# Kernel optimization log

Measured on AMD Instinct MI355X. Metric: run time of the kernel, lower is better.

The kernel has to match this reference:

```python
import jax, jax.numpy as jnp
import numpy as np

N = 100000   # nodes
E = 400000   # edges
G = 5000     # graphs (20 nodes each)
H = 128      # hidden_channels
ATOM_D, BOND_D, BOOL_D = 16, 8, 2
NODE_D = 30 + ATOM_D + 3 * BOOL_D   # 52
EDGE_D = 2 + BOND_D + 3 * BOOL_D    # 16


def setup_inputs() -> dict:
    key = jax.random.key(0)
    ks = jax.random.split(key, 24)
    rn = lambda k, shape: jax.random.normal(k, shape, dtype=jnp.float32) * 0.05
    # node features: [atom_idx, 10 continuous, 3 bools]
    atom_idx = jax.random.randint(ks[0], (N,), 1, 119)
    node_cont = jax.random.normal(ks[1], (N, 10), dtype=jnp.float32)
    node_bool = jax.random.randint(ks[2], (N, 3), 0, 2)
    x = jnp.concatenate([atom_idx[:, None].astype(jnp.float32), node_cont,
                         node_bool.astype(jnp.float32)], axis=1)
    # edge features: [bond_idx, 1 continuous, 3 bools]
    bond_idx = jax.random.randint(ks[3], (E,), 1, 22)
    edge_cont = jax.random.normal(ks[4], (E, 1), dtype=jnp.float32)
    edge_bool = jax.random.randint(ks[5], (E, 3), 0, 2)
    edge_attr = jnp.concatenate([bond_idx[:, None].astype(jnp.float32), edge_cont,
                                 edge_bool.astype(jnp.float32)], axis=1)
    edge_index = jax.random.randint(ks[6], (2, E), 0, N)
    batch = jnp.repeat(jnp.arange(G, dtype=jnp.int32), N // G)
    # embeddings (with padding rows zeroed, as nn.Embedding padding_idx)
    atom_emb = rn(ks[7], (119, ATOM_D)).at[0].set(0.0)
    bond_emb = rn(ks[8], (22, BOND_D)).at[0].set(0.0)
    bool_emb = rn(ks[9], (3, BOOL_D)).at[2].set(0.0)
    Wn = rn(ks[10], (10, 30)); bn = jnp.zeros((30,), jnp.float32)
    We = rn(ks[11], (1, 2));   be = jnp.zeros((2,), jnp.float32)
    Wl1 = rn(ks[12], (NODE_D, H)); bl1 = jnp.zeros((H,), jnp.float32)
    Wr1 = rn(ks[13], (NODE_D, H)); br1 = jnp.zeros((H,), jnp.float32)
    Wedge1 = rn(ks[14], (EDGE_D, H)); att1 = rn(ks[15], (H,))
    bias1 = jnp.zeros((H,), jnp.float32)
    Wl2 = rn(ks[16], (H, H)); bl2 = jnp.zeros((H,), jnp.float32)
    Wr2 = rn(ks[17], (H, H)); br2 = jnp.zeros((H,), jnp.float32)
    Wedge2 = rn(ks[18], (EDGE_D, H)); att2 = rn(ks[19], (H,))
    bias2 = jnp.zeros((H,), jnp.float32)
    return dict(x=x, edge_index=edge_index, edge_attr=edge_attr, batch=batch,
                atom_emb=atom_emb, bond_emb=bond_emb, bool_emb=bool_emb,
                Wn=Wn, bn=bn, We=We, be=be,
                Wl1=Wl1, bl1=bl1, Wr1=Wr1, br1=br1, Wedge1=Wedge1, att1=att1, bias1=bias1,
                Wl2=Wl2, bl2=bl2, Wr2=Wr2, br2=br2, Wedge2=Wedge2, att2=att2, bias2=bias2)


def _gatv2(h, src, dst, e_lin, Wl, bl, Wr, br, att, bias):
    # PyG GATv2Conv, heads=1: xl = lin_l(x) (source), xr = lin_r(x) (target)
    xl = h @ Wl + bl
    xr = h @ Wr + br
    m = xl[src] + xr[dst] + e_lin                      # [E', H]
    a = jax.nn.leaky_relu(m, 0.2) @ att                # [E']
    amax = jax.ops.segment_max(a, dst, num_segments=N)
    ex = jnp.exp(a - amax[dst])
    denom = jax.ops.segment_sum(ex, dst, num_segments=N)
    alpha = ex / denom[dst]                            # softmax over incoming edges
    out = jax.ops.segment_sum(alpha[:, None] * xl[src], dst, num_segments=N)
    return out + bias


def reference(x, edge_index, edge_attr, batch,
              atom_emb, bond_emb, bool_emb, Wn, bn, We, be,
              Wl1, bl1, Wr1, br1, Wedge1, att1, bias1,
              Wl2, bl2, Wr2, br2, Wedge2, att2, bias2):
    # --- encode nodes ---
    ai = x[:, 0].astype(jnp.int32)
    nb = x[:, 11:14].astype(jnp.int32)
    h = jnp.concatenate([atom_emb[ai], x[:, 1:11] @ Wn + bn,
                         bool_emb[nb[:, 0]], bool_emb[nb[:, 1]], bool_emb[nb[:, 2]]], axis=1)
    # --- encode edges ---
    bi = edge_attr[:, 0].astype(jnp.int32)
    eb = edge_attr[:, 2:5].astype(jnp.int32)
    e = jnp.concatenate([bond_emb[bi], edge_attr[:, 1:2] @ We + be,
                         bool_emb[eb[:, 0]], bool_emb[eb[:, 1]], bool_emb[eb[:, 2]]], axis=1)
    src, dst = edge_index[0], edge_index[1]
    # --- add self loops with fill_value='mean' (mean of in-edge attrs per node) ---
    cnt = jax.ops.segment_sum(jnp.ones((E,), h.dtype), dst, num_segments=N)
    loop_attr = jax.ops.segment_sum(e, dst, num_segments=N) / jnp.maximum(cnt, 1.0)[:, None]
    e_full = jnp.concatenate([e, loop_attr], axis=0)          # [E+N, EDGE_D]
    loop = jnp.arange(N, dtype=src.dtype)
    src_f = jnp.concatenate([src, loop])
    dst_f = jnp.concatenate([dst, loop])
    # --- 3 GATv2 layers (layers 2 and 3 share weights, as in the original) ---
    h = jax.nn.relu(_gatv2(h, src_f, dst_f, e_full @ Wedge1, Wl1, bl1, Wr1, br1, att1, bias1))
    e_lin2 = e_full @ Wedge2
    h = jax.nn.relu(_gatv2(h, src_f, dst_f, e_lin2, Wl2, bl2, Wr2, br2, att2, bias2))
    h = jax.nn.relu(_gatv2(h, src_f, dst_f, e_lin2, Wl2, bl2, Wr2, br2, att2, bias2))
    # --- global_max_pool readout ---
    return jax.ops.segment_max(h, batch, num_segments=G)
```

## Files before the change

### kernel.cpp

```cpp
#include <hip/hip_runtime.h>
#include <hip/hip_fp16.h>

#define N_NODES 100000
#define N_EDGES 400000
#define N_GRAPHS 5000
#define NPG 20
#define SCAN_NB 256
#define SCAN_CHUNK ((N_NODES + SCAN_NB - 1) / SCAN_NB)
#define TAB_STRIDE (256 * 128 + 128)
#define F1 8192
#define F2 16384
#define NB_ENC ((N_NODES + 255) / 256)
#define NB_HIST ((N_EDGES + 255) / 256)

typedef __attribute__((ext_vector_type(8))) _Float16 f16x8;
typedef __attribute__((ext_vector_type(2))) _Float16 h2;
typedef __attribute__((ext_vector_type(4))) float f32x4;

#define DPP_QUAD_XOR1 0xB1
#define DPP_QUAD_XOR2 0x4E
#define DPP_ROW_HALF_MIRROR 0x141
#define DPP_ROW_MIRROR 0x140
template <int CTRL>
__device__ __forceinline__ float dpp_add(float x) {
  int p = __builtin_amdgcn_update_dpp(0, __float_as_int(x), CTRL, 0xf, 0xf, true);
  return x + __int_as_float(p);
}

__global__ __launch_bounds__(256) void k_prologue(
    const float* __restrict__ x, const float* __restrict__ atom_emb,
    const float* __restrict__ bool_emb, const float* __restrict__ Wn,
    const float* __restrict__ bn, __half* __restrict__ h0,
    const int* __restrict__ dst, int* __restrict__ cnt,
    const float* __restrict__ Wedge1, const float* __restrict__ Wedge2,
    const float* __restrict__ bond_emb, const float* __restrict__ We,
    const float* __restrict__ be, __half* __restrict__ tabs,
    const float* __restrict__ Wl1, const float* __restrict__ Wr1,
    const float* __restrict__ Wl2, const float* __restrict__ Wr2,
    unsigned short* __restrict__ fr, int* __restrict__ ghist) {
  int b = blockIdx.x, tid = threadIdx.x;
  if (b < NB_ENC) {
    int n = b * 256 + tid;
    if (n >= N_NODES) return;
    const float* xr = x + (size_t)n * 14;
    int ai = (int)xr[0];
    _Float16 hr[64];
    #pragma unroll
    for (int j = 0; j < 16; j++) hr[j] = (_Float16)atom_emb[ai * 16 + j];
    float xc[10];
    #pragma unroll
    for (int k = 0; k < 10; k++) xc[k] = xr[1 + k];
    #pragma unroll
    for (int c = 0; c < 30; c++) {
      float s = bn[c];
      #pragma unroll
      for (int k = 0; k < 10; k++) s += xc[k] * Wn[k * 30 + c];
      hr[16 + c] = (_Float16)s;
    }
    #pragma unroll
    for (int t = 0; t < 3; t++) {
      int bb = (int)xr[11 + t];
      hr[46 + 2 * t]     = (_Float16)bool_emb[2 * bb];
      hr[46 + 2 * t + 1] = (_Float16)bool_emb[2 * bb + 1];
    }
    #pragma unroll
    for (int j = 52; j < 64; j++) hr[j] = (_Float16)0.0f;
    uint4* d4 = (uint4*)(h0 + (size_t)n * 64);
    const uint4* s4 = (const uint4*)hr;
    #pragma unroll
    for (int j = 0; j < 8; j++) d4[j] = s4[j];
  } else if (b < NB_ENC + NB_HIST) {
    int e = (b - NB_ENC) * 256 + tid;
    if (e >= N_EDGES) return;
    atomicAdd(cnt + dst[e], 1);
  } else if (b == NB_ENC + NB_HIST) {
    if (tid < 64) ghist[tid] = 0;
    int s = tid >> 7, c = tid & 127;
    const float* W = s ? Wedge2 : Wedge1;
    __half* T12 = tabs + (size_t)s * TAB_STRIDE;
    __half* v   = T12 + 256 * 128;
    float w8 = W[8 * 128 + c], w9 = W[9 * 128 + c];
    v[c] = __float2half(We[0] * w8 + We[1] * w9);
    float cst = be[0] * w8 + be[1] * w9;
    float bond[22];
    for (int bb = 0; bb < 22; bb++) {
      float acc = 0.f;
      #pragma unroll
      for (int k = 0; k < 8; k++) acc += bond_emb[bb * 8 + k] * W[k * 128 + c];
      bond[bb] = acc;
    }
    for (int combo = 0; combo < 8; combo++) {
      float t2 = cst;
      #pragma unroll
      for (int tt = 0; tt < 3; tt++) {
        int bt = (combo >> tt) & 1;
        t2 += bool_emb[bt * 2 + 0] * W[(10 + 2 * tt + 0) * 128 + c];
        t2 += bool_emb[bt * 2 + 1] * W[(10 + 2 * tt + 1) * 128 + c];
      }
      for (int bb = 0; bb < 22; bb++)
        T12[(combo * 32 + bb) * 128 + c] = __float2half(bond[bb] + t2);
      for (int bb = 22; bb < 32; bb++)
        T12[(combo * 32 + bb) * 128 + c] = __float2half(0.f);
    }
  } else {
    int g = (b - (NB_ENC + NB_HIST + 1)) * 256 + tid;
    const float* W; int K; unsigned short* base; int fl;
    if (g < 1024)      { W = Wl1; K = 52;  base = fr;               fl = g; }
    else if (g < 2048) { W = Wr1; K = 52;  base = fr + F1;          fl = g - 1024; }
    else if (g < 4096) { W = Wl2; K = 128; base = fr + 2 * F1;      fl = g - 2048; }
    else if (g < 6144) { W = Wr2; K = 128; base = fr + 2 * F1 + F2; fl = g - 4096; }
    else return;
    int l = fl & 63, ctn = fl >> 6;
    int tn = ctn & 7, c = ctn >> 3;
    int n = tn * 16 + (l & 15);
    int kb = c * 32 + (l >> 4) * 8;
    unsigned h8[8];
    #pragma unroll
    for (int j = 0; j < 8; j++) {
      int k = kb + j;
      float v = (k < K) ? W[(size_t)k * 128 + n] : 0.f;
      __half hv = __float2half(v);
      h8[j] = (unsigned)*(unsigned short*)&hv;
    }
    uint4 hv4 = make_uint4(h8[0] | (h8[1] << 16), h8[2] | (h8[3] << 16),
                           h8[4] | (h8[5] << 16), h8[6] | (h8[7] << 16));
    *(uint4*)(base + (size_t)fl * 8) = hv4;
  }
}

__global__ __launch_bounds__(256) void k_scan1(const int* __restrict__ cnt,
                                               int* __restrict__ bsum,
                                               int* __restrict__ ghist) {
  __shared__ int red[256];
  __shared__ int lh[64];
  int b = blockIdx.x, t = threadIdx.x;
  if (t < 64) lh[t] = 0;
  __syncthreads();
  int beg = b * SCAN_CHUNK;
  int end = beg + SCAN_CHUNK; if (end > N_NODES) end = N_NODES;
  int s = 0;
  for (int i = beg + t; i < end; i += 256) {
    int cv = cnt[i];
    s += cv + 1;
    atomicAdd(&lh[cv < 63 ? cv : 63], 1);
  }
  red[t] = s;
  __syncthreads();
  for (int off = 128; off > 0; off >>= 1) {
    if (t < off) red[t] += red[t + off];
    __syncthreads();
  }
  if (t == 0) bsum[b] = red[0];
  if (t < 64 && lh[t] > 0) atomicAdd(&ghist[t], lh[t]);
}

__global__ __launch_bounds__(256) void k_scan3(const int* __restrict__ cnt,
                                               const int* __restrict__ bsum,
                                               int* __restrict__ indptr,
                                               int* __restrict__ cursor,
                                               const int* __restrict__ ghist,
                                               int* __restrict__ gcur) {
  __shared__ int sh[256];
  __shared__ int carry;
  int b = blockIdx.x, t = threadIdx.x;
  sh[t] = bsum[t];
  __syncthreads();
  for (int off = 1; off < 256; off <<= 1) {
    int v = (t >= off) ? sh[t - off] : 0;
    __syncthreads();
    sh[t] += v;
    __syncthreads();
  }
  if (t == 0) carry = (b > 0) ? sh[b - 1] : 0;
  __syncthreads();
  int beg = b * SCAN_CHUNK;
  int end = beg + SCAN_CHUNK; if (end > N_NODES) end = N_NODES;
  for (int base = beg; base < end; base += 256) {
    int i = base + t;
    int v = (i < end) ? cnt[i] + 1 : 0;
    sh[t] = v;
    __syncthreads();
    for (int off = 1; off < 256; off <<= 1) {
      int u = (t >= off) ? sh[t - off] : 0;
      __syncthreads();
      sh[t] += u;
      __syncthreads();
    }
    int excl = sh[t] - v;
    if (i < end) {
      int val = carry + excl;
      indptr[i] = val;
      cursor[i] = val;
    }
    __syncthreads();
    if (t == 255) carry += sh[255];
    __syncthreads();
  }
  if (b == 0 && t == 0) indptr[N_NODES] = N_EDGES + N_NODES;
  if (b == 0) {
    __syncthreads();
    if (t < 64) sh[t] = ghist[t];
    __syncthreads();
    if (t == 0) {
      int run = 0;
      for (int i = 0; i < 64; i++) { int v = sh[i]; sh[i] = run; run += v; }
    }
    __syncthreads();
    if (t < 64) gcur[t] = sh[t];
  }
}

__global__ void k_fill(const int* __restrict__ srcA,
                       const int* __restrict__ dst,
                       const float* __restrict__ eattr,
                       int* __restrict__ cursor,
                       int2* __restrict__ scode,
                       const int* __restrict__ cnt,
                       int* __restrict__ gcur,
                       int* __restrict__ perm) {
  int b = blockIdx.x, t = threadIdx.x;
  if (b < NB_HIST) {
    int e = b * 256 + t;
    if (e >= N_EDGES) return;
    const float* r = eattr + (size_t)e * 5;
    int bi = (int)r[0];
    float ec = r[1];
    int combo = (int)r[2] + 2 * (int)r[3] + 4 * (int)r[4];
    unsigned meta = (unsigned)(bi | (combo << 5));
    __half hec = __float2half(ec);
    meta |= ((unsigned)*(unsigned short*)&hec) << 16;
    int d = dst[e];
    int p = atomicAdd(&cursor[d], 1);
    scode[p] = make_int2(srcA[e], (int)meta);
  } else {
    __shared__ int lh[64];
    __shared__ int lbase[64];
    if (t < 64) lh[t] = 0;
    __syncthreads();
    int n = (b - NB_HIST) * 256 + t;
    bool v = (n < N_NODES);
    int dc = 0, r = 0;
    if (v) {
      int cv = cnt[n];
      dc = cv < 63 ? cv : 63;
      r = atomicAdd(&lh[dc], 1);
    }
    __syncthreads();
    if (t < 64 && lh[t] > 0) lbase[t] = atomicAdd(&gcur[t], lh[t]);
    __syncthreads();
    if (v) perm[lbase[dc] + r] = n;
  }
}

template <int KPAD>
__global__ __launch_bounds__(256, 4) void k_gemm2m(const __half* __restrict__ A,
                                                   const unsigned short* __restrict__ WfL,
                                                   const unsigned short* __restrict__ WfR,
                                                   const float* __restrict__ bl_,
                                                   const float* __restrict__ br_,
                                                   __half* __restrict__ outl,
                                                   __half* __restrict__ outr) {
  __shared__ unsigned short Bs[2][8192];
  const int tid = threadIdx.x;
  const int wv = tid >> 6, lane = tid & 63;
  const int tw = blockIdx.x * 4 + wv;
  const bool active = (tw < N_NODES / 16);
  const int ml = lane & 15, q = lane >> 4;
  const int m0 = active ? tw * 16 : 0;
  f32x4 accL[8], accR[8];
  #pragma unroll
  for (int t = 0; t < 8; t++) {
    accL[t] = (f32x4){0.f, 0.f, 0.f, 0.f};
    accR[t] = (f32x4){0.f, 0.f, 0.f, 0.f};
  }
  const _Float16* ar0 = (const _Float16*)A + (size_t)(m0 + ml) * KPAD + q * 8;
  constexpr int NC2 = KPAD / 64;
  for (int c2 = 0; c2 < NC2; c2++) {
    #pragma unroll
    for (int i0 = 0; i0 < 1024; i0 += 256) {
      int i = i0 + tid;
      size_t g = ((size_t)c2 * 1024 + i) * 8;
      *(uint4*)(&Bs[0][i * 8]) = *(const uint4*)(WfL + g);
      *(uint4*)(&Bs[1][i * 8]) = *(const uint4*)(WfR + g);
    }
    __syncthreads();
    #pragma unroll
    for (int sub = 0; sub < 2; sub++) {
      f16x8 a = *(const f16x8*)(ar0 + c2 * 64 + sub * 32);
      #pragma unroll
      for (int t = 0; t < 8; t++) {
        int idx = (sub * 512 + t * 64 + lane) * 8;
        f16x8 bL = *(const f16x8*)(&Bs[0][idx]);
        f16x8 bR = *(const f16x8*)(&Bs[1][idx]);
        accL[t] = __builtin_amdgcn_mfma_f32_16x16x32_f16(a, bL, accL[t], 0, 0, 0);
        accR[t] = __builtin_amdgcn_mfma_f32_16x16x32_f16(a, bR, accR[t], 0, 0, 0);
      }
    }
    __syncthreads();
  }
  __syncthreads();
  if (!active) return;
  __half* eb = (__half*)&Bs[0][0] + wv * 2048;
  const int srow = q * 4;
  const int rrow0 = lane >> 4;
  const int rcol = (lane & 15) * 8;
  #pragma unroll
  for (int t = 0; t < 8; t++) {
    int n = t * 16 + ml;
    float bL = bl_[n];
    #pragma unroll
    for (int r = 0; r < 4; r++)
      eb[(srow + r) * 128 + n] = __float2half(accL[t][r] + bL);
  }
  #pragma unroll
  for (int pp = 0; pp < 4; pp++) {
    uint4 v = *(const uint4*)(eb + pp * 512 + lane * 8);
    *(uint4*)(outl + (size_t)(m0 + pp * 4 + rrow0) * 128 + rcol) = v;
  }
  #pragma unroll
  for (int t = 0; t < 8; t++) {
    int n = t * 16 + ml;
    float bR = br_[n];
    #pragma unroll
    for (int r = 0; r < 4; r++)
      eb[(srow + r) * 128 + n] = __float2half(accR[t][r] + bR);
  }
  #pragma unroll
  for (int pp = 0; pp < 4; pp++) {
    uint4 v = *(const uint4*)(eb + pp * 512 + lane * 8);
    *(uint4*)(outr + (size_t)(m0 + pp * 4 + rrow0) * 128 + rcol) = v;
  }
}

__global__ __launch_bounds__(256) void k_gat(const __half* __restrict__ xl,
                                             const __half* __restrict__ xr,
                                             const int* __restrict__ indptr,
                                             const int2* __restrict__ scode,
                                             const __half* __restrict__ tabs,
                                             const float* __restrict__ att,
                                             const float* __restrict__ bias,
                                             __half* __restrict__ hout,
                                             const int* __restrict__ perm) {
  int wid = (blockIdx.x * 256 + threadIdx.x) >> 6;
  int nw = (gridDim.x * 256) >> 6;
  int lane = threadIdx.x & 63;
  int q4 = lane >> 4;
  int c = (lane & 15) * 8;
  const __half* T12 = tabs;
  uint4 vu_ = *(const uint4*)(tabs + 256 * 128 + c);
  h2 v4[4] = {*reinterpret_cast<h2*>(&vu_.x), *reinterpret_cast<h2*>(&vu_.y),
              *reinterpret_cast<h2*>(&vu_.z), *reinterpret_cast<h2*>(&vu_.w)};
  float4 af0 = *(const float4*)(att + c);
  float4 af1 = *(const float4*)(att + c + 4);
  h2 a4[4] = {{(_Float16)af0.x, (_Float16)af0.y}, {(_Float16)af0.z, (_Float16)af0.w},
              {(_Float16)af1.x, (_Float16)af1.y}, {(_Float16)af1.z, (_Float16)af1.w}};
  float bb[8];
  {
    float4 b0 = *(const float4*)(bias + c);
    float4 b1 = *(const float4*)(bias + c + 4);
    bb[0] = b0.x; bb[1] = b0.y; bb[2] = b0.z; bb[3] = b0.w;
    bb[4] = b1.x; bb[5] = b1.y; bb[6] = b1.z; bb[7] = b1.w;
  }
  const h2 z2 = {(_Float16)0.f, (_Float16)0.f};
  const h2 k2 = {(_Float16)0.2f, (_Float16)0.2f};
  wid = __builtin_amdgcn_readfirstlane(wid);
  const int stride = nw * 4;
  int nb = wid * 4;
  if (nb >= N_NODES) return;
  int n = perm[(N_NODES - 4 - nb) + q4];
  int bg = indptr[n], en = indptr[n + 1];
  uint4 xru = *(const uint4*)(xr + (size_t)n * 128 + c);
  while (true) {
    int nb2 = nb + stride;
    bool has2 = (nb2 < N_NODES);
    int n2 = has2 ? perm[(N_NODES - 4 - nb2) + q4] : n;
    int bg2 = indptr[n2];
    int en2 = indptr[n2 + 1];
    uint4 xru2 = *(const uint4*)(xr + (size_t)n2 * 128 + c);
    int beg = bg, end1 = en - 1;
    h2 xrv[4] = {*reinterpret_cast<h2*>(&xru.x), *reinterpret_cast<h2*>(&xru.y),
                 *reinterpret_cast<h2*>(&xru.z), *reinterpret_cast<h2*>(&xru.w)};
    float denom = 0.f;
    float acc[8] = {0.f, 0.f, 0.f, 0.f, 0.f, 0.f, 0.f, 0.f};
    h2 els[4] = {z2, z2, z2, z2};
    int d = end1 - beg;
    int dmax = d, m2;
    m2 = __shfl_xor(dmax, 16, 64); dmax = dmax > m2 ? dmax : m2;
    m2 = __shfl_xor(dmax, 32, 64); dmax = dmax > m2 ? dmax : m2;
    bool uni = __all(d == dmax) != 0;

    auto EDGE1 = [&](int jj) {
      int2 sc = scode[jj];
      uint4 lv = *(const uint4*)(xl + (size_t)sc.x * 128 + c);
      uint4 tv = *(const uint4*)(T12 + (size_t)(sc.y & 255) * 128 + c);
      unsigned short us = (unsigned short)((unsigned)sc.y >> 16);
      _Float16 eh = *reinterpret_cast<_Float16*>(&us);
      h2 xl4[4] = {*reinterpret_cast<h2*>(&lv.x), *reinterpret_cast<h2*>(&lv.y),
                   *reinterpret_cast<h2*>(&lv.z), *reinterpret_cast<h2*>(&lv.w)};
      h2 t4[4] = {*reinterpret_cast<h2*>(&tv.x), *reinterpret_cast<h2*>(&tv.y),
                  *reinterpret_cast<h2*>(&tv.z), *reinterpret_cast<h2*>(&tv.w)};
      h2 eh2 = {eh, eh};
      h2 dd = z2;
      #pragma unroll
      for (int k = 0; k < 4; k++) {
        h2 el = eh2 * v4[k] + t4[k];
        h2 m = xl4[k] + xrv[k] + el;
        h2 l = __builtin_elementwise_max(m, z2) + k2 * __builtin_elementwise_min(m, z2);
        dd += l * a4[k];
        els[k] += el;
      }
      float tt = (float)dd[0] + (float)dd[1];
      tt = dpp_add<DPP_QUAD_XOR1>(tt);
      tt = dpp_add<DPP_QUAD_XOR2>(tt);
      tt = dpp_add<DPP_ROW_HALF_MIRROR>(tt);
      tt = dpp_add<DPP_ROW_MIRROR>(tt);
      float ex = __expf(tt);
      denom += ex;
      #pragma unroll
      for (int k = 0; k < 4; k++) {
        acc[2 * k]     += ex * (float)xl4[k][0];
        acc[2 * k + 1] += ex * (float)xl4[k][1];
      }
    };

    if (uni) {
      int fullit = dmax >> 2, rem = dmax & 3;
      for (int it = 0; it < fullit; it++) {
        int j = beg + it * 4;
        int2 sc4[4]; uint4 lv[4]; uint4 tv[4];
        #pragma unroll
        for (int u = 0; u < 4; u++) sc4[u] = scode[j + u];
        #pragma unroll
        for (int u = 0; u < 4; u++)
          lv[u] = *(const uint4*)(xl + (size_t)sc4[u].x * 128 + c);
        #pragma unroll
        for (int u = 0; u < 4; u++)
          tv[u] = *(const uint4*)(T12 + (size_t)(sc4[u].y & 255) * 128 + c);
        float tt[4]; h2 xlv[4][4];
        #pragma unroll
        for (int u = 0; u < 4; u++) {
          xlv[u][0] = *reinterpret_cast<h2*>(&lv[u].x);
          xlv[u][1] = *reinterpret_cast<h2*>(&lv[u].y);
          xlv[u][2] = *reinterpret_cast<h2*>(&lv[u].z);
          xlv[u][3] = *reinterpret_cast<h2*>(&lv[u].w);
          h2 t4[4] = {*reinterpret_cast<h2*>(&tv[u].x), *reinterpret_cast<h2*>(&tv[u].y),
                      *reinterpret_cast<h2*>(&tv[u].z), *reinterpret_cast<h2*>(&tv[u].w)};
          unsigned short us = (unsigned short)((unsigned)sc4[u].y >> 16);
          _Float16 eh = *reinterpret_cast<_Float16*>(&us);
          h2 eh2 = {eh, eh};
          h2 dd = z2;
          #pragma unroll
          for (int k = 0; k < 4; k++) {
            h2 el = eh2 * v4[k] + t4[k];
            h2 m = xlv[u][k] + xrv[k] + el;
            h2 l = __builtin_elementwise_max(m, z2) + k2 * __builtin_elementwise_min(m, z2);
            dd += l * a4[k];
            els[k] += el;
          }
          tt[u] = (float)dd[0] + (float)dd[1];
        }
        #pragma unroll
        for (int u = 0; u < 4; u++) tt[u] = dpp_add<DPP_QUAD_XOR1>(tt[u]);
        #pragma unroll
        for (int u = 0; u < 4; u++) tt[u] = dpp_add<DPP_QUAD_XOR2>(tt[u]);
        #pragma unroll
        for (int u = 0; u < 4; u++) tt[u] = dpp_add<DPP_ROW_HALF_MIRROR>(tt[u]);
        #pragma unroll
        for (int u = 0; u < 4; u++) tt[u] = dpp_add<DPP_ROW_MIRROR>(tt[u]);
        #pragma unroll
        for (int u = 0; u < 4; u++) {
          float ex = __expf(tt[u]);
          denom += ex;
          #pragma unroll
          for (int k = 0; k < 4; k++) {
            acc[2 * k]     += ex * (float)xlv[u][k][0];
            acc[2 * k + 1] += ex * (float)xlv[u][k][1];
          }
        }
      }
      int j = beg + fullit * 4;
      if (rem > 0) EDGE1(j);
      if (rem > 1) EDGE1(j + 1);
      if (rem > 2) EDGE1(j + 2);
    } else {
      int last = (end1 > beg) ? end1 - 1 : beg;
      int iters = (dmax + 3) >> 2;
      for (int it = 0; it < iters; it++) {
        int j = beg + it * 4;
        int2 sc4[4]; h2 xlv[4][4]; float tt[4];
        bool val[4];
        #pragma unroll
        for (int u = 0; u < 4; u++) {
          val[u] = (j + u < end1);
          int jj = val[u] ? j + u : last;
          sc4[u] = scode[jj];
        }
        #pragma unroll
        for (int u = 0; u < 4; u++) {
          int s = val[u] ? sc4[u].x : n;
          uint4 lv = *(const uint4*)(xl + (size_t)s * 128 + c);
          xlv[u][0] = *reinterpret_cast<h2*>(&lv.x);
          xlv[u][1] = *reinterpret_cast<h2*>(&lv.y);
          xlv[u][2] = *reinterpret_cast<h2*>(&lv.z);
          xlv[u][3] = *reinterpret_cast<h2*>(&lv.w);
        }
        #pragma unroll
        for (int u = 0; u < 4; u++) {
          int meta = val[u] ? (sc4[u].y & 255) : 255;
          unsigned short us = val[u] ? (unsigned short)((unsigned)sc4[u].y >> 16)
                                     : (unsigned short)0;
          _Float16 eh = *reinterpret_cast<_Float16*>(&us);
          uint4 tv = *(const uint4*)(T12 + (size_t)meta * 128 + c);
          h2 t4[4] = {*reinterpret_cast<h2*>(&tv.x), *reinterpret_cast<h2*>(&tv.y),
                      *reinterpret_cast<h2*>(&tv.z), *reinterpret_cast<h2*>(&tv.w)};
          h2 eh2 = {eh, eh};
          h2 dd = z2;
          #pragma unroll
          for (int k = 0; k < 4; k++) {
            h2 el = eh2 * v4[k] + t4[k];
            h2 m = xlv[u][k] + xrv[k] + el;
            h2 l = __builtin_elementwise_max(m, z2) + k2 * __builtin_elementwise_min(m, z2);
            dd += l * a4[k];
            els[k] += el;
          }
          tt[u] = (float)dd[0] + (float)dd[1];
        }
        #pragma unroll
        for (int u = 0; u < 4; u++) tt[u] = dpp_add<DPP_QUAD_XOR1>(tt[u]);
        #pragma unroll
        for (int u = 0; u < 4; u++) tt[u] = dpp_add<DPP_QUAD_XOR2>(tt[u]);
        #pragma unroll
        for (int u = 0; u < 4; u++) tt[u] = dpp_add<DPP_ROW_HALF_MIRROR>(tt[u]);
        #pragma unroll
        for (int u = 0; u < 4; u++) tt[u] = dpp_add<DPP_ROW_MIRROR>(tt[u]);
        #pragma unroll
        for (int u = 0; u < 4; u++) {
          float ex = val[u] ? __expf(tt[u]) : 0.f;
          denom += ex;
          #pragma unroll
          for (int k = 0; k < 4; k++) {
            acc[2 * k]     += ex * (float)xlv[u][k][0];
            acc[2 * k + 1] += ex * (float)xlv[u][k][1];
          }
        }
      }
    }
    int cntn = d;
    float inv_cnt = 1.0f / (float)(cntn > 0 ? cntn : 1);
    uint4 xnu = *(const uint4*)(xl + (size_t)n * 128 + c);
    h2 xn[4] = {*reinterpret_cast<h2*>(&xnu.x), *reinterpret_cast<h2*>(&xnu.y),
                *reinterpret_cast<h2*>(&xnu.z), *reinterpret_cast<h2*>(&xnu.w)};
    float afv[8] = {af0.x, af0.y, af0.z, af0.w, af1.x, af1.y, af1.z, af1.w};
    float ts = 0.f;
    float xnf[8];
    #pragma unroll
    for (int k = 0; k < 4; k++) {
      #pragma unroll
      for (int hh = 0; hh < 2; hh++) {
        int i = 2 * k + hh;
        xnf[i] = (float)xn[k][hh];
        float m = xnf[i] + (float)xrv[k][hh] + (float)els[k][hh] * inv_cnt;
        float l = m > 0.f ? m : 0.2f * m;
        ts += l * afv[i];
      }
    }
    ts = dpp_add<DPP_QUAD_XOR1>(ts);
    ts = dpp_add<DPP_QUAD_XOR2>(ts);
    ts = dpp_add<DPP_ROW_HALF_MIRROR>(ts);
    ts = dpp_add<DPP_ROW_MIRROR>(ts);
    float ex = __expf(ts);
    denom += ex;
    #pragma unroll
    for (int i = 0; i < 8; i++) acc[i] += ex * xnf[i];
    float invd = 1.0f / denom;
    h2 p[4];
    #pragma unroll
    for (int k = 0; k < 4; k++) {
      float o0 = acc[2 * k] * invd + bb[2 * k];
      float o1 = acc[2 * k + 1] * invd + bb[2 * k + 1];
      o0 = o0 > 0.f ? o0 : 0.f;
      o1 = o1 > 0.f ? o1 : 0.f;
      p[k] = (h2){(_Float16)o0, (_Float16)o1};
    }
    uint4 st = make_uint4(*reinterpret_cast<unsigned*>(&p[0]),
                          *reinterpret_cast<unsigned*>(&p[1]),
                          *reinterpret_cast<unsigned*>(&p[2]),
                          *reinterpret_cast<unsigned*>(&p[3]));
    *(uint4*)(hout + (size_t)n * 128 + c) = st;
    if (!has2) break;
    nb = nb2; n = n2; bg = bg2; en = en2; xru = xru2;
  }
}

__global__ void k_readout(const __half* __restrict__ h, float* __restrict__ out) {
  int wid = (blockIdx.x * blockDim.x + threadIdx.x) >> 6;
  int lane = threadIdx.x & 63;
  if (wid >= N_GRAPHS) return;
  int c = lane * 2;
  float m0 = -1e30f, m1 = -1e30f;
  for (int i = 0; i < NPG; i++) {
    unsigned v = *(const unsigned*)(h + ((size_t)(wid * NPG + i)) * 128 + c);
    h2 f = *reinterpret_cast<h2*>(&v);
    m0 = fmaxf(m0, (float)f[0]);
    m1 = fmaxf(m1, (float)f[1]);
  }
  float2 o; o.x = m0; o.y = m1;
  *(float2*)(out + (size_t)wid * 128 + c) = o;
}

extern "C" void kernel_launch(void* const* d_in, const int* in_sizes, int n_in,
                              void* d_out, int out_size, void* d_ws, size_t ws_size,
                              hipStream_t stream) {
  (void)in_sizes; (void)n_in; (void)out_size; (void)ws_size;
  const float* x        = (const float*)d_in[0];
  const int*   eindex   = (const int*)d_in[1];
  const float* eattr    = (const float*)d_in[2];
  const float* atom_emb = (const float*)d_in[4];
  const float* bond_emb = (const float*)d_in[5];
  const float* bool_emb = (const float*)d_in[6];
  const float* Wn   = (const float*)d_in[7];
  const float* bn   = (const float*)d_in[8];
  const float* We   = (const float*)d_in[9];
  const float* be   = (const float*)d_in[10];
  const float* Wl1  = (const float*)d_in[11];
  const float* bl1  = (const float*)d_in[12];
  const float* Wr1  = (const float*)d_in[13];
  const float* br1  = (const float*)d_in[14];
  const float* Wedge1 = (const float*)d_in[15];
  const float* att1 = (const float*)d_in[16];
  const float* bias1 = (const float*)d_in[17];
  const float* Wl2  = (const float*)d_in[18];
  const float* bl2  = (const float*)d_in[19];
  const float* Wr2  = (const float*)d_in[20];
  const float* br2  = (const float*)d_in[21];
  const float* Wedge2 = (const float*)d_in[22];
  const float* att2 = (const float*)d_in[23];
  const float* bias2 = (const float*)d_in[24];

  const int* srcA = eindex;
  const int* dstA = eindex + N_EDGES;

  char* p = (char*)d_ws;
  auto alloc = [&](size_t bytes) {
    char* r = p;
    p += (bytes + 255) & ~(size_t)255;
    return r;
  };
  __half* h0     = (__half*)alloc((size_t)N_NODES * 64 * 2);
  __half* h      = (__half*)alloc((size_t)N_NODES * 128 * 2);
  __half* xl     = (__half*)alloc((size_t)N_NODES * 128 * 2);
  __half* xrb    = (__half*)alloc((size_t)N_NODES * 128 * 2);
  int*    cnt    = (int*)alloc((size_t)N_NODES * 4);
  int*    indptr = (int*)alloc((size_t)(N_NODES + 1) * 4);
  int*    cursor = (int*)alloc((size_t)N_NODES * 4);
  int2*   scode  = (int2*)alloc((size_t)(N_EDGES + N_NODES) * 8);
  __half* tabs   = (__half*)alloc((size_t)2 * TAB_STRIDE * 2);
  unsigned short* wfrag = (unsigned short*)alloc((size_t)(2 * F1 + 2 * F2) * 2);
  int*    bsum   = (int*)alloc((size_t)SCAN_NB * 4);
  int*    ghist  = (int*)alloc((size_t)64 * 4);
  int*    gcur   = (int*)alloc((size_t)64 * 4);
  int*    perm   = (int*)alloc((size_t)N_NODES * 4);

  (void)hipMemsetAsync(cnt, 0, (size_t)N_NODES * 4, stream);

  k_prologue<<<NB_ENC + NB_HIST + 1 + 24, 256, 0, stream>>>(
      x, atom_emb, bool_emb, Wn, bn, h0, dstA, cnt,
      Wedge1, Wedge2, bond_emb, We, be, tabs,
      Wl1, Wr1, Wl2, Wr2, wfrag, ghist);
  k_scan1<<<SCAN_NB, 256, 0, stream>>>(cnt, bsum, ghist);
  k_scan3<<<SCAN_NB, 256, 0, stream>>>(cnt, bsum, indptr, cursor, ghist, gcur);
  k_fill<<<NB_HIST + NB_ENC, 256, 0, stream>>>(srcA, dstA, eattr, cursor, scode,
                                               cnt, gcur, perm);

  const unsigned short* f_l1 = wfrag;
  const unsigned short* f_r1 = wfrag + F1;
  const unsigned short* f_l2 = wfrag + 2 * F1;
  const unsigned short* f_r2 = wfrag + 2 * F1 + F2;

  const int GB2 = (N_NODES / 16 + 3) / 4;

  k_gemm2m<64><<<GB2, 256, 0, stream>>>(h0, f_l1, f_r1, bl1, br1, xl, xrb);
  k_gat<<<2048, 256, 0, stream>>>(xl, xrb, indptr, scode, tabs, att1, bias1, h, perm);

  k_gemm2m<128><<<GB2, 256, 0, stream>>>(h, f_l2, f_r2, bl2, br2, xl, xrb);
  k_gat<<<2048, 256, 0, stream>>>(xl, xrb, indptr, scode, tabs + TAB_STRIDE, att2, bias2, h, perm);

  k_gemm2m<128><<<GB2, 256, 0, stream>>>(h, f_l2, f_r2, bl2, br2, xl, xrb);
  k_gat<<<2048, 256, 0, stream>>>(xl, xrb, indptr, scode, tabs + TAB_STRIDE, att2, bias2, h, perm);

  k_readout<<<(N_GRAPHS * 64 + 255) / 256, 256, 0, stream>>>(h, (float*)d_out);
}
```

Measured before the change: 325.5 us.

## Store node features in degree-sorted order to make GAT row accesses contiguous

Node feature rows (h0, xl, xr, h) are now stored in the degree-bucketed permutation order instead of original node order. Edge source indices are remapped through an inverse permutation, and readout gathers through it too. This is meant to make the GAT kernel's per-node reads and writes of xr, xl and h sequential rather than scattered. In exchange it adds a separate permutation kernel launch, moves the node encoder after the permutation is built, and makes readout reads indirect.

Result: slower. 343.1 us (+5.4%).

```diff
diff --git a/kernel.cpp b/kernel.cpp
--- a/kernel.cpp
+++ b/kernel.cpp
@@ -28,9 +28,7 @@
 }
 
 __global__ __launch_bounds__(256) void k_prologue(
-    const float* __restrict__ x, const float* __restrict__ atom_emb,
-    const float* __restrict__ bool_emb, const float* __restrict__ Wn,
-    const float* __restrict__ bn, __half* __restrict__ h0,
+    const float* __restrict__ bool_emb,
     const int* __restrict__ dst, int* __restrict__ cnt,
     const float* __restrict__ Wedge1, const float* __restrict__ Wedge2,
     const float* __restrict__ bond_emb, const float* __restrict__ We,
@@ -39,41 +37,11 @@
     const float* __restrict__ Wl2, const float* __restrict__ Wr2,
     unsigned short* __restrict__ fr, int* __restrict__ ghist) {
   int b = blockIdx.x, tid = threadIdx.x;
-  if (b < NB_ENC) {
-    int n = b * 256 + tid;
-    if (n >= N_NODES) return;
-    const float* xr = x + (size_t)n * 14;
-    int ai = (int)xr[0];
-    _Float16 hr[64];
-    #pragma unroll
-    for (int j = 0; j < 16; j++) hr[j] = (_Float16)atom_emb[ai * 16 + j];
-    float xc[10];
-    #pragma unroll
-    for (int k = 0; k < 10; k++) xc[k] = xr[1 + k];
-    #pragma unroll
-    for (int c = 0; c < 30; c++) {
-      float s = bn[c];
-      #pragma unroll
-      for (int k = 0; k < 10; k++) s += xc[k] * Wn[k * 30 + c];
-      hr[16 + c] = (_Float16)s;
-    }
-    #pragma unroll
-    for (int t = 0; t < 3; t++) {
-      int bb = (int)xr[11 + t];
-      hr[46 + 2 * t]     = (_Float16)bool_emb[2 * bb];
-      hr[46 + 2 * t + 1] = (_Float16)bool_emb[2 * bb + 1];
-    }
-    #pragma unroll
-    for (int j = 52; j < 64; j++) hr[j] = (_Float16)0.0f;
-    uint4* d4 = (uint4*)(h0 + (size_t)n * 64);
-    const uint4* s4 = (const uint4*)hr;
-    #pragma unroll
-    for (int j = 0; j < 8; j++) d4[j] = s4[j];
-  } else if (b < NB_ENC + NB_HIST) {
-    int e = (b - NB_ENC) * 256 + tid;
+  if (b < NB_HIST) {
+    int e = b * 256 + tid;
     if (e >= N_EDGES) return;
     atomicAdd(cnt + dst[e], 1);
-  } else if (b == NB_ENC + NB_HIST) {
+  } else if (b == NB_HIST) {
     if (tid < 64) ghist[tid] = 0;
     int s = tid >> 7, c = tid & 127;
     const float* W = s ? Wedge2 : Wedge1;
@@ -103,7 +71,7 @@
         T12[(combo * 32 + bb) * 128 + c] = __float2half(0.f);
     }
   } else {
-    int g = (b - (NB_ENC + NB_HIST + 1)) * 256 + tid;
+    int g = (b - (NB_HIST + 1)) * 256 + tid;
     const float* W; int K; unsigned short* base; int fl;
     if (g < 1024)      { W = Wl1; K = 52;  base = fr;               fl = g; }
     else if (g < 2048) { W = Wr1; K = 52;  base = fr + F1;          fl = g - 1024; }
@@ -210,14 +178,44 @@
   }
 }
 
-__global__ void k_fill(const int* __restrict__ srcA,
-                       const int* __restrict__ dst,
-                       const float* __restrict__ eattr,
-                       int* __restrict__ cursor,
-                       int2* __restrict__ scode,
-                       const int* __restrict__ cnt,
-                       int* __restrict__ gcur,
-                       int* __restrict__ perm) {
+__global__ void k_perm(const int* __restrict__ cnt, int* __restrict__ gcur,
+                       int* __restrict__ perm, int* __restrict__ iperm) {
+  __shared__ int lh[64];
+  __shared__ int lbase[64];
+  int b = blockIdx.x, t = threadIdx.x;
+  if (t < 64) lh[t] = 0;
+  __syncthreads();
+  int n = b * 256 + t;
+  bool v = (n < N_NODES);
+  int dc = 0, r = 0;
+  if (v) {
+    int cv = cnt[n];
+    dc = cv < 63 ? cv : 63;
+    r = atomicAdd(&lh[dc], 1);
+  }
+  __syncthreads();
+  if (t < 64 && lh[t] > 0) lbase[t] = atomicAdd(&gcur[t], lh[t]);
+  __syncthreads();
+  if (v) {
+    int pos = lbase[dc] + r;
+    perm[pos] = n;
+    iperm[n] = pos;
+  }
+}
+
+__global__ void k_fill2(const int* __restrict__ srcA,
+                        const int* __restrict__ dst,
+                        const float* __restrict__ eattr,
+                        int* __restrict__ cursor,
+                        int2* __restrict__ scode,
+                        const int* __restrict__ iperm,
+                        const float* __restrict__ x,
+                        const float* __restrict__ atom_emb,
+                        const float* __restrict__ bool_emb,
+                        const float* __restrict__ Wn,
+                        const float* __restrict__ bn,
+                        const int* __restrict__ perm,
+                        __half* __restrict__ h0) {
   int b = blockIdx.x, t = threadIdx.x;
   if (b < NB_HIST) {
     int e = b * 256 + t;
@@ -231,24 +229,38 @@
     meta |= ((unsigned)*(unsigned short*)&hec) << 16;
     int d = dst[e];
     int p = atomicAdd(&cursor[d], 1);
-    scode[p] = make_int2(srcA[e], (int)meta);
+    scode[p] = make_int2(iperm[srcA[e]], (int)meta);
   } else {
-    __shared__ int lh[64];
-    __shared__ int lbase[64];
-    if (t < 64) lh[t] = 0;
-    __syncthreads();
-    int n = (b - NB_HIST) * 256 + t;
-    bool v = (n < N_NODES);
-    int dc = 0, r = 0;
-    if (v) {
-      int cv = cnt[n];
-      dc = cv < 63 ? cv : 63;
-      r = atomicAdd(&lh[dc], 1);
-    }
-    __syncthreads();
-    if (t < 64 && lh[t] > 0) lbase[t] = atomicAdd(&gcur[t], lh[t]);
-    __syncthreads();
-    if (v) perm[lbase[dc] + r] = n;
+    int i = (b - NB_HIST) * 256 + t;
+    if (i >= N_NODES) return;
+    int n = perm[i];
+    const float* xr = x + (size_t)n * 14;
+    int ai = (int)xr[0];
+    _Float16 hr[64];
+    #pragma unroll
+    for (int j = 0; j < 16; j++) hr[j] = (_Float16)atom_emb[ai * 16 + j];
+    float xc[10];
+    #pragma unroll
+    for (int k = 0; k < 10; k++) xc[k] = xr[1 + k];
+    #pragma unroll
+    for (int c = 0; c < 30; c++) {
+      float s = bn[c];
+      #pragma unroll
+      for (int k = 0; k < 10; k++) s += xc[k] * Wn[k * 30 + c];
+      hr[16 + c] = (_Float16)s;
+    }
+    #pragma unroll
+    for (int tt = 0; tt < 3; tt++) {
+      int bb = (int)xr[11 + tt];
+      hr[46 + 2 * tt]     = (_Float16)bool_emb[2 * bb];
+      hr[46 + 2 * tt + 1] = (_Float16)bool_emb[2 * bb + 1];
+    }
+    #pragma unroll
+    for (int j = 52; j < 64; j++) hr[j] = (_Float16)0.0f;
+    uint4* d4 = (uint4*)(h0 + (size_t)i * 64);
+    const uint4* s4 = (const uint4*)hr;
+    #pragma unroll
+    for (int j = 0; j < 8; j++) d4[j] = s4[j];
   }
 }
 
@@ -367,16 +379,18 @@
   const int stride = nw * 4;
   int nb = wid * 4;
   if (nb >= N_NODES) return;
-  int n = perm[(N_NODES - 4 - nb) + q4];
-  int bg = indptr[n], en = indptr[n + 1];
-  uint4 xru = *(const uint4*)(xr + (size_t)n * 128 + c);
+  int row = (N_NODES - 4 - nb) + q4;
+  int n0 = perm[row];
+  int bg = indptr[n0], en = indptr[n0 + 1];
+  uint4 xru = *(const uint4*)(xr + (size_t)row * 128 + c);
   while (true) {
     int nb2 = nb + stride;
     bool has2 = (nb2 < N_NODES);
-    int n2 = has2 ? perm[(N_NODES - 4 - nb2) + q4] : n;
-    int bg2 = indptr[n2];
-    int en2 = indptr[n2 + 1];
-    uint4 xru2 = *(const uint4*)(xr + (size_t)n2 * 128 + c);
+    int row2 = has2 ? (N_NODES - 4 - nb2) + q4 : row;
+    int np = perm[row2];
+    int bg2 = indptr[np];
+    int en2 = indptr[np + 1];
+    uint4 xru2 = *(const uint4*)(xr + (size_t)row2 * 128 + c);
     int beg = bg, end1 = en - 1;
     h2 xrv[4] = {*reinterpret_cast<h2*>(&xru.x), *reinterpret_cast<h2*>(&xru.y),
                  *reinterpret_cast<h2*>(&xru.z), *reinterpret_cast<h2*>(&xru.w)};
@@ -497,7 +511,7 @@
         }
         #pragma unroll
         for (int u = 0; u < 4; u++) {
-          int s = val[u] ? sc4[u].x : n;
+          int s = val[u] ? sc4[u].x : row;
           uint4 lv = *(const uint4*)(xl + (size_t)s * 128 + c);
           xlv[u][0] = *reinterpret_cast<h2*>(&lv.x);
           xlv[u][1] = *reinterpret_cast<h2*>(&lv.y);
@@ -547,7 +561,7 @@
     }
     int cntn = d;
     float inv_cnt = 1.0f / (float)(cntn > 0 ? cntn : 1);
-    uint4 xnu = *(const uint4*)(xl + (size_t)n * 128 + c);
+    uint4 xnu = *(const uint4*)(xl + (size_t)row * 128 + c);
     h2 xn[4] = {*reinterpret_cast<h2*>(&xnu.x), *reinterpret_cast<h2*>(&xnu.y),
                 *reinterpret_cast<h2*>(&xnu.z), *reinterpret_cast<h2*>(&xnu.w)};
     float afv[8] = {af0.x, af0.y, af0.z, af0.w, af1.x, af1.y, af1.z, af1.w};
@@ -586,20 +600,23 @@
                           *reinterpret_cast<unsigned*>(&p[1]),
                           *reinterpret_cast<unsigned*>(&p[2]),
                           *reinterpret_cast<unsigned*>(&p[3]));
-    *(uint4*)(hout + (size_t)n * 128 + c) = st;
+    *(uint4*)(hout + (size_t)row * 128 + c) = st;
     if (!has2) break;
-    nb = nb2; n = n2; bg = bg2; en = en2; xru = xru2;
-  }
-}
-
-__global__ void k_readout(const __half* __restrict__ h, float* __restrict__ out) {
+    nb = nb2; row = row2; bg = bg2; en = en2; xru = xru2;
+  }
+}
+
+__global__ void k_readout(const __half* __restrict__ h,
+                          const int* __restrict__ iperm,
+                          float* __restrict__ out) {
   int wid = (blockIdx.x * blockDim.x + threadIdx.x) >> 6;
   int lane = threadIdx.x & 63;
   if (wid >= N_GRAPHS) return;
   int c = lane * 2;
   float m0 = -1e30f, m1 = -1e30f;
   for (int i = 0; i < NPG; i++) {
-    unsigned v = *(const unsigned*)(h + ((size_t)(wid * NPG + i)) * 128 + c);
+    int row = iperm[wid * NPG + i];
+    unsigned v = *(const unsigned*)(h + (size_t)row * 128 + c);
     h2 f = *reinterpret_cast<h2*>(&v);
     m0 = fmaxf(m0, (float)f[0]);
     m1 = fmaxf(m1, (float)f[1]);
@@ -660,17 +677,20 @@
   int*    ghist  = (int*)alloc((size_t)64 * 4);
   int*    gcur   = (int*)alloc((size_t)64 * 4);
   int*    perm   = (int*)alloc((size_t)N_NODES * 4);
+  int*    iperm  = (int*)alloc((size_t)N_NODES * 4);
 
   (void)hipMemsetAsync(cnt, 0, (size_t)N_NODES * 4, stream);
 
-  k_prologue<<<NB_ENC + NB_HIST + 1 + 24, 256, 0, stream>>>(
-      x, atom_emb, bool_emb, Wn, bn, h0, dstA, cnt,
+  k_prologue<<<NB_HIST + 1 + 24, 256, 0, stream>>>(
+      bool_emb, dstA, cnt,
       Wedge1, Wedge2, bond_emb, We, be, tabs,
       Wl1, Wr1, Wl2, Wr2, wfrag, ghist);
   k_scan1<<<SCAN_NB, 256, 0, stream>>>(cnt, bsum, ghist);
   k_scan3<<<SCAN_NB, 256, 0, stream>>>(cnt, bsum, indptr, cursor, ghist, gcur);
-  k_fill<<<NB_HIST + NB_ENC, 256, 0, stream>>>(srcA, dstA, eattr, cursor, scode,
-                                               cnt, gcur, perm);
+  k_perm<<<NB_ENC, 256, 0, stream>>>(cnt, gcur, perm, iperm);
+  k_fill2<<<NB_HIST + NB_ENC, 256, 0, stream>>>(srcA, dstA, eattr, cursor, scode,
+                                                iperm, x, atom_emb, bool_emb,
+                                                Wn, bn, perm, h0);
 
   const unsigned short* f_l1 = wfrag;
   const unsigned short* f_r1 = wfrag + F1;
@@ -688,5 +708,5 @@
   k_gemm2m<128><<<GB2, 256, 0, stream>>>(h, f_l2, f_r2, bl2, br2, xl, xrb);
   k_gat<<<2048, 256, 0, stream>>>(xl, xrb, indptr, scode, tabs + TAB_STRIDE, att2, bias2, h, perm);
 
-  k_readout<<<(N_GRAPHS * 64 + 255) / 256, 256, 0, stream>>>(h, (float*)d_out);
-}
+  k_readout<<<(N_GRAPHS * 64 + 255) / 256, 256, 0, stream>>>(h, iperm, (float*)d_out);
+}
```
